# Performance work log

Hardware: AMD Instinct MI355X
Metric: run time of the kernel (lower is better)

The kernel has to match this reference:

```python
import jax, jax.numpy as jnp
import numpy as np

DIM = 2048
H = 16
HD = 128
S = 2640          # frame_seq_len(22*40=880) * num_frame_per_block(3)
CACHE = 5280      # 6 cached frames
MAXPOS = 8192
EPS = 1e-6


def rmsnorm(x, g, eps=EPS):
    return x * jax.lax.rsqrt(jnp.mean(x * x, axis=-1, keepdims=True) + eps) * g


def apply_rope_interleaved(x, cos, sin):
    # x: [s, H, HD]; cos/sin: [s, HD//2]; is_neox=False -> adjacent pairs
    x1 = x[..., 0::2]
    x2 = x[..., 1::2]
    c = cos[:, None, :]
    s_ = sin[:, None, :]
    o1 = x1 * c - x2 * s_
    o2 = x2 * c + x1 * s_
    return jnp.stack([o1, o2], axis=-1).reshape(x.shape)


def setup_inputs() -> dict:
    key = jax.random.key(0)
    ks = jax.random.split(key, 10)
    w_scale = DIM ** -0.5
    x = jax.random.normal(ks[0], (1, S, DIM), dtype=jnp.float32)
    # cos_sin_cache: [max_pos, HD] = [cos(HD//2) | sin(HD//2)], real rope values
    inv_freq = 1.0 / (10000.0 ** (np.arange(0, HD, 2, dtype=np.float32) / HD))
    t = np.arange(MAXPOS, dtype=np.float32)
    ang = np.outer(t, inv_freq)  # [MAXPOS, HD//2]
    freqs = jnp.asarray(np.concatenate([np.cos(ang), np.sin(ang)], axis=1), dtype=jnp.float32)
    k_cache = jax.random.normal(ks[1], (CACHE, H, HD), dtype=jnp.float32)
    v_cache = jax.random.normal(ks[2], (CACHE, H, HD), dtype=jnp.float32)
    Wq = jax.random.normal(ks[3], (DIM, DIM), dtype=jnp.float32) * w_scale
    Wk = jax.random.normal(ks[4], (DIM, DIM), dtype=jnp.float32) * w_scale
    Wv = jax.random.normal(ks[5], (DIM, DIM), dtype=jnp.float32) * w_scale
    Wo = jax.random.normal(ks[6], (DIM, DIM), dtype=jnp.float32) * w_scale
    bq = jnp.zeros((DIM,), jnp.float32)
    bk = jnp.zeros((DIM,), jnp.float32)
    bv = jnp.zeros((DIM,), jnp.float32)
    bo = jnp.zeros((DIM,), jnp.float32)
    gq = jnp.ones((DIM,), jnp.float32)
    gk = jnp.ones((DIM,), jnp.float32)
    return {"x": x, "freqs": freqs, "k_cache": k_cache, "v_cache": v_cache,
            "Wq": Wq, "bq": bq, "Wk": Wk, "bk": bk, "Wv": Wv, "bv": bv,
            "Wo": Wo, "bo": bo, "gq": gq, "gk": gk, "current_start": CACHE}


def reference(x, freqs, k_cache, v_cache, Wq, bq, Wk, bk, Wv, bv, Wo, bo, gq, gk, current_start):
    s = x.shape[1]
    xf = x[0]                                   # [s, DIM], B==1
    q = rmsnorm(xf @ Wq.T + bq, gq).reshape(s, H, HD)
    k = rmsnorm(xf @ Wk.T + bk, gk).reshape(s, H, HD)
    v = (xf @ Wv.T + bv).reshape(s, H, HD)
    # fused RoPE via cos_sin_cache lookup, interleaved (is_neox=False)
    positions = jnp.arange(s, dtype=jnp.int32) + current_start
    cs = freqs[positions]                       # [s, HD]
    cos, sin = cs[:, : HD // 2], cs[:, HD // 2:]
    rq = apply_rope_interleaved(q, cos, sin)
    rk = apply_rope_interleaved(k, cos, sin)
    # streaming attention: full access to cache, causal within incoming block
    k_all = jnp.concatenate([k_cache, rk], axis=0)  # [L, H, HD]
    v_all = jnp.concatenate([v_cache, v], axis=0)
    L = k_all.shape[0]
    scale = HD ** -0.5
    scores = jnp.einsum("qhd,khd->hqk", rq, k_all) * scale  # [H, s, L]
    kv_idx = jnp.arange(L)
    q_idx = jnp.arange(s)
    mask = (kv_idx[None, :] - (L - s)) <= q_idx[:, None]    # cache always visible
    scores = jnp.where(mask[None, :, :], scores, jnp.float32(-1e30))
    attn = jax.nn.softmax(scores, axis=-1)
    out = jnp.einsum("hqk,khd->qhd", attn, v_all).reshape(s, DIM)
    y = out @ Wo.T + bo
    return y[None]                              # [1, s, DIM]
```

## Files before the change

### kernel.cpp

```cpp
#include <hip/hip_runtime.h>

#define DIMN 2048
#define NH 16
#define HDIM 128

typedef __attribute__((ext_vector_type(4))) float f32x4;
typedef __attribute__((ext_vector_type(8))) __bf16 bfx8;
typedef __attribute__((ext_vector_type(4))) __bf16 bf16x4;
typedef __attribute__((ext_vector_type(8))) unsigned short u16x8;

__device__ __forceinline__ unsigned short f2bf(float f){
  unsigned u = __builtin_bit_cast(unsigned, f);
  u += 0x7fffu + ((u >> 16) & 1u);
  return (unsigned short)(u >> 16);
}
__device__ __forceinline__ float bf2f(unsigned short h){
  unsigned u = (unsigned)h << 16;
  return __builtin_bit_cast(float, u);
}

__device__ __forceinline__ void gl_lds16(const void* g, void* l){
  __builtin_amdgcn_global_load_lds((const __attribute__((address_space(1))) void*)g,
                                   (__attribute__((address_space(3))) void*)l, 16, 0, 0);
}

#define MFMA16(a,b,c) __builtin_amdgcn_mfma_f32_16x16x32_bf16((a),(b),(c),0,0,0)

__global__ __launch_bounds__(256) void cast_bf16_kernel(const float* __restrict__ in,
                                                        unsigned short* __restrict__ out, int n8){
  int i = blockIdx.x*256 + threadIdx.x;
  if (i >= n8) return;
  const float4* p = (const float4*)(in + (size_t)i*8);
  float4 a = p[0], b = p[1];
  u16x8 o;
  o[0]=f2bf(a.x); o[1]=f2bf(a.y); o[2]=f2bf(a.z); o[3]=f2bf(a.w);
  o[4]=f2bf(b.x); o[5]=f2bf(b.y); o[6]=f2bf(b.z); o[7]=f2bf(b.w);
  *(u16x8*)(out + (size_t)i*8) = o;
}

__global__ __launch_bounds__(256) void kcache_kernel(const float* __restrict__ kc,
                                                     unsigned short* __restrict__ kb,
                                                     int R, int L_){
  const int gid = blockIdx.x*256 + threadIdx.x;
  if (gid >= R*256) return;
  const size_t idx = (size_t)gid * 8;
  const int k   = (int)(idx >> 11);
  const int rem = (int)(idx & 2047);
  const int hh  = rem >> 7, d = rem & 127;
  const float4* p = (const float4*)(kc + idx);
  float4 a = p[0], b = p[1];
  u16x8 o;
  o[0]=f2bf(a.x); o[1]=f2bf(a.y); o[2]=f2bf(a.z); o[3]=f2bf(a.w);
  o[4]=f2bf(b.x); o[5]=f2bf(b.y); o[6]=f2bf(b.z); o[7]=f2bf(b.w);
  *(u16x8*)(kb + (size_t)hh*L_*HDIM + (size_t)k*HDIM + d) = o;
}

__global__ __launch_bounds__(256) void vtrans_kernel(const float* __restrict__ src,
                                                     unsigned short* __restrict__ vt,
                                                     int R, int koff, int L_){
  __shared__ __align__(16) unsigned short tile[32][72];
  const int kb0 = blockIdx.x * 64, db0 = blockIdx.y * 32, hh = blockIdx.z;
  const int t = threadIdx.x;
  const int kk = t >> 2, dd = (t & 3) * 8;
  const int k = kb0 + kk;
  if (k < R){
    const float* p = src + (size_t)k*DIMN + hh*HDIM + db0 + dd;
    float4 a = ((const float4*)p)[0], b = ((const float4*)p)[1];
    tile[dd+0][kk] = f2bf(a.x); tile[dd+1][kk] = f2bf(a.y);
    tile[dd+2][kk] = f2bf(a.z); tile[dd+3][kk] = f2bf(a.w);
    tile[dd+4][kk] = f2bf(b.x); tile[dd+5][kk] = f2bf(b.y);
    tile[dd+6][kk] = f2bf(b.z); tile[dd+7][kk] = f2bf(b.w);
  }
  __syncthreads();
  const int d = t >> 3, k0 = (t & 7) * 8;
  unsigned short* dst = vt + (size_t)hh*HDIM*L_ + (size_t)(db0+d)*L_ + koff + kb0 + k0;
  if (kb0 + k0 + 8 <= R){
    *(u16x8*)dst = *(const u16x8*)&tile[d][k0];
  } else {
    #pragma unroll
    for (int e=0;e<8;++e) if (kb0 + k0 + e < R) dst[e] = tile[d][k0+e];
  }
}

__global__ __launch_bounds__(256) void vtrans_bf16_kernel(const unsigned short* __restrict__ src,
    unsigned short* __restrict__ vt, int R, int koff, int L_){
  __shared__ __align__(16) unsigned short tile[32][72];
  const int kb0 = blockIdx.x * 64, db0 = blockIdx.y * 32, hh = blockIdx.z;
  const int t = threadIdx.x;
  const int kk = t >> 2, dd = (t & 3) * 8;
  const int k = kb0 + kk;
  if (k < R){
    u16x8 a = *(const u16x8*)(src + (size_t)k*DIMN + hh*HDIM + db0 + dd);
    #pragma unroll
    for (int e=0;e<8;++e) tile[dd+e][kk] = a[e];
  }
  __syncthreads();
  const int d = t >> 3, k0 = (t & 7) * 8;
  unsigned short* dst = vt + (size_t)hh*HDIM*L_ + (size_t)(db0+d)*L_ + koff + kb0 + k0;
  if (kb0 + k0 + 8 <= R){
    *(u16x8*)dst = *(const u16x8*)&tile[d][k0];
  } else {
    #pragma unroll
    for (int e=0;e<8;++e) if (kb0 + k0 + e < R) dst[e] = tile[d][k0+e];
  }
}

__global__ __launch_bounds__(256) void norm_rope_kernel(const unsigned short* __restrict__ lin,
    const float* __restrict__ g, const float* __restrict__ freqs, const int* __restrict__ cur,
    unsigned short* __restrict__ out, int S_, size_t head_stride, int row_off, float oscale){
  const int q = blockIdx.x, t = threadIdx.x;
  u16x8 v = *(const u16x8*)(lin + (size_t)q*DIMN + t*8);
  float x[8];
  #pragma unroll
  for (int e=0;e<8;++e) x[e] = bf2f(v[e]);
  float ss = 0.f;
  #pragma unroll
  for (int e=0;e<8;++e) ss += x[e]*x[e];
  for (int m=1;m<64;m<<=1) ss += __shfl_xor(ss, m);
  __shared__ float red[4];
  if ((t & 63) == 0) red[t>>6] = ss;
  __syncthreads();
  const float tot = red[0]+red[1]+red[2]+red[3];
  const float rstd = rsqrtf(tot * (1.0f/2048.0f) + 1e-6f);
  const int n0 = t*8;
  float xr[8];
  #pragma unroll
  for (int e=0;e<8;++e) xr[e] = x[e] * rstd * g[n0+e];
  const int pos = cur[0] + q;
  const int hh = n0 >> 7, d0 = n0 & 127;
  const float* fr = freqs + (size_t)pos * HDIM;
  float o[8];
  #pragma unroll
  for (int p=0;p<4;++p){
    const int j = (d0>>1) + p;
    const float c = fr[j], s = fr[64+j];
    o[2*p]   = xr[2*p]*c - xr[2*p+1]*s;
    o[2*p+1] = xr[2*p+1]*c + xr[2*p]*s;
  }
  u16x8 ov;
  #pragma unroll
  for (int e=0;e<8;++e) ov[e] = f2bf(o[e]*oscale);
  *(u16x8*)(out + (size_t)hh*head_stride + (size_t)(q+row_off)*HDIM + d0) = ov;
}

__global__ __launch_bounds__(256,2) void gemm_bt(const unsigned short* __restrict__ A,
    const unsigned short* __restrict__ B, const float* __restrict__ bias,
    float* __restrict__ C, int M, int N, int K){
  __shared__ __align__(16) unsigned short As[128*64];
  __shared__ __align__(16) unsigned short Bs[128*64];
  const int t = threadIdx.x;
  const int w = t >> 6, lane = t & 63, lh = lane >> 4, ll = lane & 15;
  const int wr = w >> 1, wc = w & 1;
  const int m0 = blockIdx.y * 128, n0 = blockIdx.x * 128;
  const int srow = t >> 3;
  const int scb  = (t & 7) * 16;
  const int swc  = (scb ^ ((srow & 7) << 4)) >> 1;
  int arow[4]; size_t brow[4];
  #pragma unroll
  for (int c=0;c<4;++c){
    int r = m0 + c*32 + srow; if (r >= M) r = M-1;
    arow[c] = r;
    brow[c] = (size_t)(n0 + c*32 + srow);
  }
  const int xsw = (ll & 7) << 4;
  f32x4 acc[4][4] = {};
  const int nk = K >> 6;
  for (int kt = 0; kt < nk; ++kt){
    const int k0 = kt << 6;
    #pragma unroll
    for (int c=0;c<4;++c){
      gl_lds16(A + (size_t)arow[c]*K + k0 + swc, (char*)As + c*4096 + w*1024);
      gl_lds16(B + brow[c]*K       + k0 + swc, (char*)Bs + c*4096 + w*1024);
    }
    asm volatile("s_waitcnt vmcnt(0)" ::: "memory");
    __syncthreads();
    #pragma unroll
    for (int kk=0;kk<2;++kk){
      const int cb = kk*64 + lh*16;
      bfx8 a[4], b[4];
      #pragma unroll
      for (int i=0;i<4;++i)
        a[i] = *(const bfx8*)((const char*)As + (wr*64 + i*16 + ll)*128 + (cb ^ xsw));
      #pragma unroll
      for (int j=0;j<4;++j)
        b[j] = *(const bfx8*)((const char*)Bs + (wc*64 + j*16 + ll)*128 + (cb ^ xsw));
      #pragma unroll
      for (int i=0;i<4;++i)
        #pragma unroll
        for (int j=0;j<4;++j)
          acc[i][j] = MFMA16(a[i], b[j], acc[i][j]);
    }
    __syncthreads();
  }
  #pragma unroll
  for (int i=0;i<4;++i){
    #pragma unroll
    for (int j=0;j<4;++j){
      const int col = n0 + wc*64 + j*16 + ll;
      const float bb = bias[col];
      #pragma unroll
      for (int r=0;r<4;++r){
        const int row = m0 + wr*64 + i*16 + lh*4 + r;
        if (row < M) C[(size_t)row*N + col] = acc[i][j][r] + bb;
      }
    }
  }
}

__global__ __launch_bounds__(256,2) void gemm_qkv(const unsigned short* __restrict__ A,
    const unsigned short* __restrict__ B0, const unsigned short* __restrict__ B1,
    const unsigned short* __restrict__ B2, const float* __restrict__ g0,
    const float* __restrict__ g1, const float* __restrict__ g2,
    unsigned short* __restrict__ C0, unsigned short* __restrict__ C1,
    unsigned short* __restrict__ C2, int M, int N, int K){
  const int zz = blockIdx.z;
  const unsigned short* B = (zz==0) ? B0 : (zz==1) ? B1 : B2;
  const float* bias       = (zz==0) ? g0 : (zz==1) ? g1 : g2;
  unsigned short* C       = (zz==0) ? C0 : (zz==1) ? C1 : C2;
  __shared__ __align__(16) unsigned short As[128*64];
  __shared__ __align__(16) unsigned short Bs[128*64];
  const int t = threadIdx.x;
  const int w = t >> 6, lane = t & 63, lh = lane >> 4, ll = lane & 15;
  const int wr = w >> 1, wc = w & 1;
  const int m0 = blockIdx.y * 128, n0 = blockIdx.x * 128;
  const int srow = t >> 3;
  const int scb  = (t & 7) * 16;
  const int swc  = (scb ^ ((srow & 7) << 4)) >> 1;
  int arow[4]; size_t brow[4];
  #pragma unroll
  for (int c=0;c<4;++c){
    int r = m0 + c*32 + srow; if (r >= M) r = M-1;
    arow[c] = r;
    brow[c] = (size_t)(n0 + c*32 + srow);
  }
  const int xsw = (ll & 7) << 4;
  f32x4 acc[4][4] = {};
  const int nk = K >> 6;
  for (int kt = 0; kt < nk; ++kt){
    const int k0 = kt << 6;
    #pragma unroll
    for (int c=0;c<4;++c){
      gl_lds16(A + (size_t)arow[c]*K + k0 + swc, (char*)As + c*4096 + w*1024);
      gl_lds16(B + brow[c]*K       + k0 + swc, (char*)Bs + c*4096 + w*1024);
    }
    asm volatile("s_waitcnt vmcnt(0)" ::: "memory");
    __syncthreads();
    #pragma unroll
    for (int kk=0;kk<2;++kk){
      const int cb = kk*64 + lh*16;
      bfx8 a[4], b[4];
      #pragma unroll
      for (int i=0;i<4;++i)
        a[i] = *(const bfx8*)((const char*)As + (wr*64 + i*16 + ll)*128 + (cb ^ xsw));
      #pragma unroll
      for (int j=0;j<4;++j)
        b[j] = *(const bfx8*)((const char*)Bs + (wc*64 + j*16 + ll)*128 + (cb ^ xsw));
      #pragma unroll
      for (int i=0;i<4;++i)
        #pragma unroll
        for (int j=0;j<4;++j)
          acc[i][j] = MFMA16(a[i], b[j], acc[i][j]);
    }
    __syncthreads();
  }
  #pragma unroll
  for (int i=0;i<4;++i){
    #pragma unroll
    for (int j=0;j<4;++j){
      const int col = n0 + wc*64 + j*16 + ll;
      const float bb = bias[col];
      #pragma unroll
      for (int r=0;r<4;++r){
        const int row = m0 + wr*64 + i*16 + lh*4 + r;
        if (row < M) C[(size_t)row*N + col] = f2bf(acc[i][j][r] + bb);
      }
    }
  }
}

__global__ __launch_bounds__(512,4) void attn_kernel(const unsigned short* __restrict__ Q,
    const unsigned short* __restrict__ K, const unsigned short* __restrict__ VT,
    unsigned short* __restrict__ O, float* __restrict__ pacc, float* __restrict__ pml,
    int S_, int L_, int CLn, int nx, int nsplit){
  __shared__ __align__(16) unsigned short Ks[2][64*128];
  __shared__ __align__(16) unsigned short Vs[2][128*64];
  __shared__ __align__(16) unsigned short Ps[8][16*64];
  const int nwg = gridDim.x;
  const int swzid = (blockIdx.x & 7)*(nwg >> 3) + (blockIdx.x >> 3);
  const int xq = swzid % nx;
  const int rest = swzid / nx;
  const int hh = rest % NH;
  const int z  = rest / NH;
  const int q0 = xq * 128;
  const int t = threadIdx.x, w = t >> 6, lane = t & 63, lh = lane >> 4, ll = lane & 15;
  const int xsw = (ll & 7) << 4;
  char* Pw = (char*)Ps[w];
  const unsigned short* Qh = Q  + (size_t)hh*S_*HDIM;
  const unsigned short* Kh = K  + (size_t)hh*L_*HDIM;
  const unsigned short* Vh = VT + (size_t)hh*HDIM*L_;
  const int wrow0 = q0 + w*16;
  bfx8 qf[4];
  {
    int qr = wrow0 + ll; if (qr >= S_) qr = S_ - 1;
    #pragma unroll
    for (int kk=0;kk<4;++kk)
      qf[kk] = *(const bfx8*)(Qh + (size_t)qr*HDIM + kk*32 + lh*8);
  }
  f32x4 acc[8] = {};
  float m_st = -1e20f, l_st = 0.f;
  int qlast = q0 + 127; if (qlast >= S_) qlast = S_ - 1;
  const int kend = CLn + qlast + 1;
  const int nt = (kend + 63) >> 6;
  const int tps = (nt + nsplit - 1) / nsplit;
  const int t0 = z * tps;
  int t1 = t0 + tps; if (t1 > nt) t1 = nt;
  const int ksrow = t >> 4, kchunk = t & 15;
  const int vsrow = t >> 3, vchunk = t & 7;
  const int myq = wrow0 + ll;
  const int last = nt - 1;

  u16x8 kreg[2], vreg[2];
  auto load_tile = [&](int ktile){
    const int kv0 = ktile << 6;
    if (ktile == last){
      #pragma unroll
      for (int c=0;c<2;++c){
        int krow = kv0 + c*32 + ksrow; if (krow >= L_) krow = L_ - 1;
        kreg[c] = *(const u16x8*)(Kh + (size_t)krow*HDIM + kchunk*8);
      }
      int vcol = kv0 + vchunk*8; if (vcol > L_ - 8) vcol = L_ - 8;
      #pragma unroll
      for (int c=0;c<2;++c)
        vreg[c] = *(const u16x8*)(Vh + (size_t)(c*64 + vsrow)*L_ + vcol);
    } else {
      #pragma unroll
      for (int c=0;c<2;++c)
        kreg[c] = *(const u16x8*)(Kh + (size_t)(kv0 + c*32 + ksrow)*HDIM + kchunk*8);
      const int vcol = kv0 + vchunk*8;
      #pragma unroll
      for (int c=0;c<2;++c)
        vreg[c] = *(const u16x8*)(Vh + (size_t)(c*64 + vsrow)*L_ + vcol);
    }
  };
  auto stage_write = [&](int b){
    #pragma unroll
    for (int c=0;c<2;++c)
      *(u16x8*)((char*)Ks[b] + (c*32 + ksrow)*256 + ((kchunk*16) ^ ((ksrow & 7) << 4))) = kreg[c];
    #pragma unroll
    for (int c=0;c<2;++c)
      *(u16x8*)((char*)Vs[b] + (c*64 + vsrow)*128 + ((vchunk*16) ^ ((vsrow & 7) << 4))) = vreg[c];
  };

  if (t0 < t1){
    load_tile(t0);
    stage_write(0);
    if (t0 + 1 < t1) load_tile(t0 + 1);
  }
  int cur = 0;
  for (int kt = t0; kt < t1; ++kt){
    const int kv0 = kt << 6;
    __syncthreads();
    const char* Kc = (const char*)Ks[cur];
    const char* Vc = (const char*)Vs[cur];
    f32x4 sc[4] = {};
    #pragma unroll
    for (int kk=0;kk<4;++kk){
      const int cb = kk*64 + lh*16;
      #pragma unroll
      for (int j=0;j<4;++j){
        bfx8 kf = *(const bfx8*)(Kc + (j*16 + ll)*256 + (cb ^ xsw));
        sc[j] = MFMA16(kf, qf[kk], sc[j]);
      }
    }
    if (kt + 1 < t1){
      stage_write(cur ^ 1);
      if (kt + 2 < t1) load_tile(kt + 2);
    }
    if (kv0 + 63 > CLn + wrow0){
      const int lim = CLn + myq;
      #pragma unroll
      for (int j=0;j<4;++j)
        #pragma unroll
        for (int r=0;r<4;++r){
          const int key = kv0 + j*16 + lh*4 + r;
          if (key > lim) sc[j][r] = -1e30f;
        }
    }
    float mt = sc[0][0];
    #pragma unroll
    for (int j=0;j<4;++j)
      #pragma unroll
      for (int r=0;r<4;++r) mt = fmaxf(mt, sc[j][r]);
    mt = fmaxf(mt, __shfl_xor(mt, 16));
    mt = fmaxf(mt, __shfl_xor(mt, 32));
    mt = fmaxf(mt, -1e20f);
    if (!__all(mt - m_st <= 11.54f)){
      const float mn = fmaxf(m_st, mt);
      const float corr = exp2f(m_st - mn);
      m_st = mn;
      l_st *= corr;
      #pragma unroll
      for (int r=0;r<4;++r){
        const float ca = __shfl(corr, lh*4 + r);
        #pragma unroll
        for (int jn=0;jn<8;++jn) acc[jn][r] *= ca;
      }
    }
    float rs = 0.f;
    #pragma unroll
    for (int j=0;j<4;++j)
      #pragma unroll
      for (int r=0;r<4;++r){
        const float pv = exp2f(sc[j][r] - m_st);
        sc[j][r] = pv;
        rs += pv;
      }
    rs += __shfl_xor(rs, 16);
    rs += __shfl_xor(rs, 32);
    l_st += rs;
    #pragma unroll
    for (int j=0;j<4;++j){
      bf16x4 pk = { (__bf16)sc[j][0], (__bf16)sc[j][1], (__bf16)sc[j][2], (__bf16)sc[j][3] };
      *(bf16x4*)(Pw + ll*128 + ((j*32 + lh*8) ^ xsw)) = pk;
    }
    #pragma unroll
    for (int kk=0;kk<2;++kk){
      const int cb = kk*64 + lh*16;
      bfx8 af = *(const bfx8*)(Pw + ll*128 + (cb ^ xsw));
      #pragma unroll
      for (int jn=0;jn<8;++jn){
        bfx8 vf = *(const bfx8*)(Vc + (jn*16 + ll)*128 + (cb ^ xsw));
        acc[jn] = MFMA16(af, vf, acc[jn]);
      }
    }
    cur ^= 1;
  }
  if (nsplit == 1){
    const float linv = 1.0f / l_st;
    #pragma unroll
    for (int r=0;r<4;++r){
      const float inv = __shfl(linv, lh*4 + r);
      const int qr = wrow0 + lh*4 + r;
      if (qr < S_){
        #pragma unroll
        for (int jn=0;jn<8;++jn)
          O[(size_t)qr*DIMN + hh*HDIM + jn*16 + ll] = f2bf(acc[jn][r]*inv);
      }
    }
  } else {
    #pragma unroll
    for (int r=0;r<4;++r){
      const int qr = wrow0 + lh*4 + r;
      if (qr < S_){
        const size_t rid = ((size_t)z*NH + hh)*S_ + qr;
        float* dst = pacc + rid*128;
        #pragma unroll
        for (int jn=0;jn<8;++jn) dst[jn*16 + ll] = acc[jn][r];
      }
    }
    if (lane < 16){
      if (myq < S_){
        const size_t rid2 = ((size_t)z*NH + hh)*S_ + myq;
        pml[rid2*2]   = m_st;
        pml[rid2*2+1] = l_st;
      }
    }
  }
}

__global__ __launch_bounds__(256) void combine_kernel(const float* __restrict__ pacc,
    const float* __restrict__ pml, unsigned short* __restrict__ ob, int S_, int nsplit){
  const int t = threadIdx.x;
  const int rid = blockIdx.x*2 + (t >> 7);
  if (rid >= S_*NH) return;
  const int d = t & 127;
  const int hh = rid / S_;
  const int q  = rid - hh*S_;
  float M = -1e20f;
  for (int s=0; s<nsplit; ++s)
    M = fmaxf(M, pml[((size_t)s*NH*S_ + rid)*2]);
  float lt = 0.f, o = 0.f;
  for (int s=0; s<nsplit; ++s){
    const float m = pml[((size_t)s*NH*S_ + rid)*2];
    const float l = pml[((size_t)s*NH*S_ + rid)*2 + 1];
    const float wgt = exp2f(m - M);
    lt += l * wgt;
    o  += pacc[((size_t)s*NH*S_ + rid)*128 + d] * wgt;
  }
  if (lt == 0.f) lt = 1.f;
  ob[(size_t)q*DIMN + hh*HDIM + d] = f2bf(o / lt);
}

extern "C" void kernel_launch(void* const* d_in, const int* in_sizes, int n_in,
                              void* d_out, int out_size, void* d_ws, size_t ws_size,
                              hipStream_t stream){
  const float* x       = (const float*)d_in[0];
  const float* freqs   = (const float*)d_in[1];
  const float* k_cache = (const float*)d_in[2];
  const float* v_cache = (const float*)d_in[3];
  const float* Wq = (const float*)d_in[4];
  const float* bq = (const float*)d_in[5];
  const float* Wk = (const float*)d_in[6];
  const float* bk = (const float*)d_in[7];
  const float* Wv = (const float*)d_in[8];
  const float* bv = (const float*)d_in[9];
  const float* Wo = (const float*)d_in[10];
  const float* bo = (const float*)d_in[11];
  const float* gq = (const float*)d_in[12];
  const float* gk = (const float*)d_in[13];
  const int*   cur = (const int*)d_in[14];

  const int S = in_sizes[0] / DIMN;
  const int CACHE_ = in_sizes[2] / DIMN;
  const int L = CACHE_ + S;
  const int CLn = L - S;

  auto al = [](size_t n){ return (n + 255) & ~(size_t)255; };
  char* base = (char*)d_ws;
  size_t off = 0;
  auto take = [&](size_t n){ char* r = base + off; off += al(n); return r; };
  unsigned short* xb  = (unsigned short*)take((size_t)S*DIMN*2);
  unsigned short* Wob = (unsigned short*)take((size_t)DIMN*DIMN*2);
  unsigned short* qb  = (unsigned short*)take((size_t)NH*S*HDIM*2);
  unsigned short* kb  = (unsigned short*)take((size_t)NH*L*HDIM*2);
  unsigned short* vtb = (unsigned short*)take((size_t)NH*HDIM*L*2);
  unsigned short* ob  = (unsigned short*)take((size_t)S*DIMN*2);
  const size_t ubase = off;
  const size_t l_sz = al((size_t)S*DIMN*2);
  const size_t w_sz = al((size_t)DIMN*DIMN*2);
  unsigned short* lin0 = (unsigned short*)(base + ubase);
  unsigned short* lin1 = (unsigned short*)(base + ubase + l_sz);
  unsigned short* lin2 = (unsigned short*)(base + ubase + 2*l_sz);
  unsigned short* Wqb  = (unsigned short*)(base + ubase + 3*l_sz);
  unsigned short* Wkb  = (unsigned short*)(base + ubase + 3*l_sz + w_sz);
  unsigned short* Wvb  = (unsigned short*)(base + ubase + 3*l_sz + 2*w_sz);
  const size_t trans_sz = 3*l_sz + 3*w_sz;
  auto pool_sz = [&](int ns){
    return al((size_t)ns*NH*S*HDIM*4) + al((size_t)ns*NH*S*2*4);
  };
  int nsplit = 1;
  if (ubase + (trans_sz > pool_sz(4) ? trans_sz : pool_sz(4)) <= ws_size) nsplit = 4;
  else if (ubase + (trans_sz > pool_sz(2) ? trans_sz : pool_sz(2)) <= ws_size) nsplit = 2;
  if (ubase + trans_sz > ws_size) return;
  float* pacc = (float*)(base + ubase);
  float* pml  = (float*)(base + ubase + al((size_t)nsplit*NH*S*HDIM*4));

  const int wn8 = DIMN*DIMN/8;
  cast_bf16_kernel<<<(S*DIMN/8+255)/256, 256, 0, stream>>>(x,  xb,  S*DIMN/8);
  cast_bf16_kernel<<<(wn8+255)/256, 256, 0, stream>>>(Wq, Wqb, wn8);
  cast_bf16_kernel<<<(wn8+255)/256, 256, 0, stream>>>(Wk, Wkb, wn8);
  cast_bf16_kernel<<<(wn8+255)/256, 256, 0, stream>>>(Wv, Wvb, wn8);
  cast_bf16_kernel<<<(wn8+255)/256, 256, 0, stream>>>(Wo, Wob, wn8);
  kcache_kernel<<<CACHE_, 256, 0, stream>>>(k_cache, kb, CACHE_, L);
  vtrans_kernel<<<dim3((CACHE_+63)/64, 4, NH), 256, 0, stream>>>(v_cache, vtb, CACHE_, 0, L);

  const int mb = (S+127)/128;
  gemm_qkv<<<dim3(DIMN/128, mb, 3), 256, 0, stream>>>(xb, Wqb, Wkb, Wvb, bq, bk, bv,
                                                      lin0, lin1, lin2, S, DIMN, DIMN);
  const float qsc = 0.08838834764831845f * 1.4426950408889634f;
  norm_rope_kernel<<<S, 256, 0, stream>>>(lin0, gq, freqs, cur, qb, S, (size_t)S*HDIM, 0, qsc);
  norm_rope_kernel<<<S, 256, 0, stream>>>(lin1, gk, freqs, cur, kb, S, (size_t)L*HDIM, CACHE_, 1.0f);
  vtrans_bf16_kernel<<<dim3((S+63)/64, 4, NH), 256, 0, stream>>>(lin2, vtb, S, CACHE_, L);

  const int nx = (S+127)/128;
  attn_kernel<<<nx*NH*nsplit, 512, 0, stream>>>(qb, kb, vtb, ob,
                                                pacc, pml, S, L, CLn, nx, nsplit);
  if (nsplit > 1)
    combine_kernel<<<(S*NH+1)/2, 256, 0, stream>>>(pacc, pml, ob, S, nsplit);
  gemm_bt<<<dim3(DIMN/128, mb), 256, 0, stream>>>(ob, Wob, bo, (float*)d_out, S, DIMN, DIMN);
}
```

Before: 524.0 us.

## Switch attention kernel to 32x32x16 MFMA with 4 waves of 32 query rows

Measured after the change: 516.8 us. No clear change (-1.4%).

```diff
diff --git a/kernel.cpp b/kernel.cpp
--- a/kernel.cpp
+++ b/kernel.cpp
@@ -5,8 +5,9 @@
 #define HDIM 128
 
 typedef __attribute__((ext_vector_type(4))) float f32x4;
+typedef __attribute__((ext_vector_type(16))) float f32x16;
 typedef __attribute__((ext_vector_type(8))) __bf16 bfx8;
-typedef __attribute__((ext_vector_type(4))) __bf16 bf16x4;
+typedef __attribute__((ext_vector_type(2))) __bf16 bf16x2;
 typedef __attribute__((ext_vector_type(8))) unsigned short u16x8;
 
 __device__ __forceinline__ unsigned short f2bf(float f){
@@ -18,6 +19,10 @@
   unsigned u = (unsigned)h << 16;
   return __builtin_bit_cast(float, u);
 }
+__device__ __forceinline__ unsigned pk2(float a, float b){
+  bf16x2 v = { (__bf16)a, (__bf16)b };
+  return __builtin_bit_cast(unsigned, v);
+}
 
 __device__ __forceinline__ void gl_lds16(const void* g, void* l){
   __builtin_amdgcn_global_load_lds((const __attribute__((address_space(1))) void*)g,
@@ -25,6 +30,7 @@
 }
 
 #define MFMA16(a,b,c) __builtin_amdgcn_mfma_f32_16x16x32_bf16((a),(b),(c),0,0,0)
+#define MFMA32(a,b,c) __builtin_amdgcn_mfma_f32_32x32x16_bf16((a),(b),(c),0,0,0)
 
 __global__ __launch_bounds__(256) void cast_bf16_kernel(const float* __restrict__ in,
                                                         unsigned short* __restrict__ out, int n8){
@@ -278,13 +284,13 @@
   }
 }
 
-__global__ __launch_bounds__(512,4) void attn_kernel(const unsigned short* __restrict__ Q,
+__global__ __launch_bounds__(256,2) void attn_kernel(const unsigned short* __restrict__ Q,
     const unsigned short* __restrict__ K, const unsigned short* __restrict__ VT,
     unsigned short* __restrict__ O, float* __restrict__ pacc, float* __restrict__ pml,
     int S_, int L_, int CLn, int nx, int nsplit){
   __shared__ __align__(16) unsigned short Ks[2][64*128];
   __shared__ __align__(16) unsigned short Vs[2][128*64];
-  __shared__ __align__(16) unsigned short Ps[8][16*64];
+  __shared__ __align__(16) unsigned short Ps[4][32*64];
   const int nwg = gridDim.x;
   const int swzid = (blockIdx.x & 7)*(nwg >> 3) + (blockIdx.x >> 3);
   const int xq = swzid % nx;
@@ -292,21 +298,23 @@
   const int hh = rest % NH;
   const int z  = rest / NH;
   const int q0 = xq * 128;
-  const int t = threadIdx.x, w = t >> 6, lane = t & 63, lh = lane >> 4, ll = lane & 15;
-  const int xsw = (ll & 7) << 4;
+  const int t = threadIdx.x, w = t >> 6, lane = t & 63;
+  const int l31 = lane & 31, h = lane >> 5;
   char* Pw = (char*)Ps[w];
+  const int xswp = (l31 & 7) << 4;
   const unsigned short* Qh = Q  + (size_t)hh*S_*HDIM;
   const unsigned short* Kh = K  + (size_t)hh*L_*HDIM;
   const unsigned short* Vh = VT + (size_t)hh*HDIM*L_;
-  const int wrow0 = q0 + w*16;
-  bfx8 qf[4];
+  const int wrow0 = q0 + w*32;
+  const int myq = wrow0 + l31;
+  bfx8 qf[8];
   {
-    int qr = wrow0 + ll; if (qr >= S_) qr = S_ - 1;
-    #pragma unroll
-    for (int kk=0;kk<4;++kk)
-      qf[kk] = *(const bfx8*)(Qh + (size_t)qr*HDIM + kk*32 + lh*8);
-  }
-  f32x4 acc[8] = {};
+    int qr = myq; if (qr >= S_) qr = S_ - 1;
+    #pragma unroll
+    for (int kk=0;kk<8;++kk)
+      qf[kk] = *(const bfx8*)(Qh + (size_t)qr*HDIM + kk*16 + h*8);
+  }
+  f32x16 acc[4] = {};
   float m_st = -1e20f, l_st = 0.f;
   int qlast = q0 + 127; if (qlast >= S_) qlast = S_ - 1;
   const int kend = CLn + qlast + 1;
@@ -316,39 +324,38 @@
   int t1 = t0 + tps; if (t1 > nt) t1 = nt;
   const int ksrow = t >> 4, kchunk = t & 15;
   const int vsrow = t >> 3, vchunk = t & 7;
-  const int myq = wrow0 + ll;
   const int last = nt - 1;
 
-  u16x8 kreg[2], vreg[2];
+  u16x8 kreg[4], vreg[4];
   auto load_tile = [&](int ktile){
     const int kv0 = ktile << 6;
     if (ktile == last){
       #pragma unroll
-      for (int c=0;c<2;++c){
-        int krow = kv0 + c*32 + ksrow; if (krow >= L_) krow = L_ - 1;
+      for (int c=0;c<4;++c){
+        int krow = kv0 + c*16 + ksrow; if (krow >= L_) krow = L_ - 1;
         kreg[c] = *(const u16x8*)(Kh + (size_t)krow*HDIM + kchunk*8);
       }
       int vcol = kv0 + vchunk*8; if (vcol > L_ - 8) vcol = L_ - 8;
       #pragma unroll
-      for (int c=0;c<2;++c)
-        vreg[c] = *(const u16x8*)(Vh + (size_t)(c*64 + vsrow)*L_ + vcol);
+      for (int c=0;c<4;++c)
+        vreg[c] = *(const u16x8*)(Vh + (size_t)(c*32 + vsrow)*L_ + vcol);
     } else {
       #pragma unroll
-      for (int c=0;c<2;++c)
-        kreg[c] = *(const u16x8*)(Kh + (size_t)(kv0 + c*32 + ksrow)*HDIM + kchunk*8);
+      for (int c=0;c<4;++c)
+        kreg[c] = *(const u16x8*)(Kh + (size_t)(kv0 + c*16 + ksrow)*HDIM + kchunk*8);
       const int vcol = kv0 + vchunk*8;
       #pragma unroll
-      for (int c=0;c<2;++c)
-        vreg[c] = *(const u16x8*)(Vh + (size_t)(c*64 + vsrow)*L_ + vcol);
+      for (int c=0;c<4;++c)
+        vreg[c] = *(const u16x8*)(Vh + (size_t)(c*32 + vsrow)*L_ + vcol);
     }
   };
   auto stage_write = [&](int b){
     #pragma unroll
-    for (int c=0;c<2;++c)
-      *(u16x8*)((char*)Ks[b] + (c*32 + ksrow)*256 + ((kchunk*16) ^ ((ksrow & 7) << 4))) = kreg[c];
-    #pragma unroll
-    for (int c=0;c<2;++c)
-      *(u16x8*)((char*)Vs[b] + (c*64 + vsrow)*128 + ((vchunk*16) ^ ((vsrow & 7) << 4))) = vreg[c];
+    for (int c=0;c<4;++c)
+      *(u16x8*)((char*)Ks[b] + (c*16 + ksrow)*256 + ((kchunk*16) ^ ((ksrow & 7) << 4))) = kreg[c];
+    #pragma unroll
+    for (int c=0;c<4;++c)
+      *(u16x8*)((char*)Vs[b] + (c*32 + vsrow)*128 + ((vchunk*16) ^ ((vsrow & 7) << 4))) = vreg[c];
   };
 
   if (t0 < t1){
@@ -356,21 +363,22 @@
     stage_write(0);
     if (t0 + 1 < t1) load_tile(t0 + 1);
   }
+  const int krow0 = l31,      koff0 = (krow0 & 7) << 4;
+  const int krow1 = 32 + l31, koff1 = (krow1 & 7) << 4;
   int cur = 0;
   for (int kt = t0; kt < t1; ++kt){
     const int kv0 = kt << 6;
     __syncthreads();
     const char* Kc = (const char*)Ks[cur];
     const char* Vc = (const char*)Vs[cur];
-    f32x4 sc[4] = {};
-    #pragma unroll
-    for (int kk=0;kk<4;++kk){
-      const int cb = kk*64 + lh*16;
-      #pragma unroll
-      for (int j=0;j<4;++j){
-        bfx8 kf = *(const bfx8*)(Kc + (j*16 + ll)*256 + (cb ^ xsw));
-        sc[j] = MFMA16(kf, qf[kk], sc[j]);
-      }
+    f32x16 sc0 = {}, sc1 = {};
+    #pragma unroll
+    for (int kk=0;kk<8;++kk){
+      const int cb = kk*32 + h*16;
+      bfx8 kf0 = *(const bfx8*)(Kc + krow0*256 + (cb ^ koff0));
+      bfx8 kf1 = *(const bfx8*)(Kc + krow1*256 + (cb ^ koff1));
+      sc0 = MFMA32(kf0, qf[kk], sc0);
+      sc1 = MFMA32(kf1, qf[kk], sc1);
     }
     if (kt + 1 < t1){
       stage_write(cur ^ 1);
@@ -379,19 +387,17 @@
     if (kv0 + 63 > CLn + wrow0){
       const int lim = CLn + myq;
       #pragma unroll
-      for (int j=0;j<4;++j)
-        #pragma unroll
-        for (int r=0;r<4;++r){
-          const int key = kv0 + j*16 + lh*4 + r;
-          if (key > lim) sc[j][r] = -1e30f;
-        }
-    }
-    float mt = sc[0][0];
-    #pragma unroll
-    for (int j=0;j<4;++j)
-      #pragma unroll
-      for (int r=0;r<4;++r) mt = fmaxf(mt, sc[j][r]);
-    mt = fmaxf(mt, __shfl_xor(mt, 16));
+      for (int r=0;r<16;++r){
+        const int kl = (r&3) + 8*(r>>2) + 4*h;
+        if (kv0 + kl      > lim) sc0[r] = -1e30f;
+        if (kv0 + 32 + kl > lim) sc1[r] = -1e30f;
+      }
+    }
+    float mt = sc0[0];
+    #pragma unroll
+    for (int r=1;r<16;++r) mt = fmaxf(mt, sc0[r]);
+    #pragma unroll
+    for (int r=0;r<16;++r) mt = fmaxf(mt, sc1[r]);
     mt = fmaxf(mt, __shfl_xor(mt, 32));
     mt = fmaxf(mt, -1e20f);
     if (!__all(mt - m_st <= 11.54f)){
@@ -400,37 +406,38 @@
       m_st = mn;
       l_st *= corr;
       #pragma unroll
-      for (int r=0;r<4;++r){
-        const float ca = __shfl(corr, lh*4 + r);
+      for (int r=0;r<16;++r){
+        const int qrow = (r&3) + 8*(r>>2) + 4*h;
+        const float ca = __shfl(corr, qrow);
         #pragma unroll
-        for (int jn=0;jn<8;++jn) acc[jn][r] *= ca;
+        for (int db=0;db<4;++db) acc[db][r] *= ca;
       }
     }
     float rs = 0.f;
     #pragma unroll
-    for (int j=0;j<4;++j)
-      #pragma unroll
-      for (int r=0;r<4;++r){
-        const float pv = exp2f(sc[j][r] - m_st);
-        sc[j][r] = pv;
-        rs += pv;
-      }
-    rs += __shfl_xor(rs, 16);
+    for (int r=0;r<16;++r){
+      const float p0 = exp2f(sc0[r] - m_st);
+      const float p1 = exp2f(sc1[r] - m_st);
+      sc0[r] = p0; sc1[r] = p1;
+      rs += p0 + p1;
+    }
     rs += __shfl_xor(rs, 32);
     l_st += rs;
     #pragma unroll
-    for (int j=0;j<4;++j){
-      bf16x4 pk = { (__bf16)sc[j][0], (__bf16)sc[j][1], (__bf16)sc[j][2], (__bf16)sc[j][3] };
-      *(bf16x4*)(Pw + ll*128 + ((j*32 + lh*8) ^ xsw)) = pk;
-    }
-    #pragma unroll
-    for (int kk=0;kk<2;++kk){
-      const int cb = kk*64 + lh*16;
-      bfx8 af = *(const bfx8*)(Pw + ll*128 + (cb ^ xsw));
-      #pragma unroll
-      for (int jn=0;jn<8;++jn){
-        bfx8 vf = *(const bfx8*)(Vc + (jn*16 + ll)*128 + (cb ^ xsw));
-        acc[jn] = MFMA16(af, vf, acc[jn]);
+    for (int r=0;r<16;r+=2){
+      const int kl = (r&3) + 8*(r>>2) + 4*h;
+      *(unsigned*)(Pw + l31*128 + ((kl*2)        ^ xswp)) = pk2(sc0[r], sc0[r+1]);
+      *(unsigned*)(Pw + l31*128 + (((kl+32)*2)   ^ xswp)) = pk2(sc1[r], sc1[r+1]);
+    }
+    #pragma unroll
+    for (int s=0;s<4;++s){
+      bfx8 pa = *(const bfx8*)(Pw + l31*128 + ((s*32 + h*16) ^ xswp));
+      const int vb = s*32 + h*16;
+      #pragma unroll
+      for (int db=0;db<4;++db){
+        const int vrow = db*32 + l31;
+        bfx8 vf = *(const bfx8*)(Vc + vrow*128 + (vb ^ ((vrow & 7) << 4)));
+        acc[db] = MFMA32(pa, vf, acc[db]);
       }
     }
     cur ^= 1;
@@ -438,32 +445,32 @@
   if (nsplit == 1){
     const float linv = 1.0f / l_st;
     #pragma unroll
-    for (int r=0;r<4;++r){
-      const float inv = __shfl(linv, lh*4 + r);
-      const int qr = wrow0 + lh*4 + r;
+    for (int r=0;r<16;++r){
+      const int qrow = (r&3) + 8*(r>>2) + 4*h;
+      const float inv = __shfl(linv, qrow);
+      const int qr = wrow0 + qrow;
       if (qr < S_){
         #pragma unroll
-        for (int jn=0;jn<8;++jn)
-          O[(size_t)qr*DIMN + hh*HDIM + jn*16 + ll] = f2bf(acc[jn][r]*inv);
+        for (int db=0;db<4;++db)
+          O[(size_t)qr*DIMN + hh*HDIM + db*32 + l31] = f2bf(acc[db][r]*inv);
       }
     }
   } else {
     #pragma unroll
-    for (int r=0;r<4;++r){
-      const int qr = wrow0 + lh*4 + r;
+    for (int r=0;r<16;++r){
+      const int qrow = (r&3) + 8*(r>>2) + 4*h;
+      const int qr = wrow0 + qrow;
       if (qr < S_){
         const size_t rid = ((size_t)z*NH + hh)*S_ + qr;
         float* dst = pacc + rid*128;
         #pragma unroll
-        for (int jn=0;jn<8;++jn) dst[jn*16 + ll] = acc[jn][r];
-      }
-    }
-    if (lane < 16){
-      if (myq < S_){
-        const size_t rid2 = ((size_t)z*NH + hh)*S_ + myq;
-        pml[rid2*2]   = m_st;
-        pml[rid2*2+1] = l_st;
-      }
+        for (int db=0;db<4;++db) dst[db*32 + l31] = acc[db][r];
+      }
+    }
+    if (lane < 32 && myq < S_){
+      const size_t rid2 = ((size_t)z*NH + hh)*S_ + myq;
+      pml[rid2*2]   = m_st;
+      pml[rid2*2+1] = l_st;
     }
   }
 }
@@ -563,7 +570,7 @@
   vtrans_bf16_kernel<<<dim3((S+63)/64, 4, NH), 256, 0, stream>>>(lin2, vtb, S, CACHE_, L);
 
   const int nx = (S+127)/128;
-  attn_kernel<<<nx*NH*nsplit, 512, 0, stream>>>(qb, kb, vtb, ob,
+  attn_kernel<<<nx*NH*nsplit, 256, 0, stream>>>(qb, kb, vtb, ob,
                                                 pacc, pml, S, L, CLn, nx, nsplit);
   if (nsplit > 1)
     combine_kernel<<<(S*NH+1)/2, 256, 0, stream>>>(pacc, pml, ob, S, nsplit);
```
